# Performance work log

Measured on AMD Instinct MI355X. Metric: run time of the kernel, lower is better.

Reference implementation:

```python
import jax, jax.numpy as jnp
import numpy as np

H = 2048       # hidden_states
T = 8192       # input sequence length
N_ACT = 4      # n_actions
IN = 3         # num_sensors / LSTM input_size


def _uniform(k, shape, scale):
    return jax.random.uniform(k, shape, jnp.float32, -scale, scale)


def setup_inputs() -> dict:
    key = jax.random.key(0)
    ks = jax.random.split(key, 12)
    s = 1.0 / np.sqrt(H)  # torch LSTM/Linear default init scale
    return {
        "x": jax.random.normal(ks[0], (T, IN), jnp.float32),
        "last_dist": jax.random.uniform(ks[1], (), jnp.float32),
        "last_heading": jax.random.uniform(ks[2], (), jnp.float32),
        "W_ih": _uniform(ks[3], (4 * H, IN), s),
        "W_hh": _uniform(ks[4], (4 * H, H), s),
        "b_ih": _uniform(ks[5], (4 * H,), s),
        "b_hh": _uniform(ks[6], (4 * H,), s),
        "W1": _uniform(ks[7], (H, 4 * H), 1.0 / np.sqrt(4 * H)),
        "b1": _uniform(ks[8], (H,), 1.0 / np.sqrt(4 * H)),
        "W2": _uniform(ks[9], (4, H), s),
        "b2": _uniform(ks[10], (4,), s),
    }


def _lstm_cell(x_gates, h, c, W_hh, b):
    # x_gates: precomputed x @ W_ih.T contribution, shape (..., 4H)
    gates = x_gates + h @ W_hh.T + b
    i, f, g, o = jnp.split(gates, 4, axis=-1)  # torch gate order i,f,g,o
    c_new = jax.nn.sigmoid(f) * c + jax.nn.sigmoid(i) * jnp.tanh(g)
    h_new = jax.nn.sigmoid(o) * jnp.tanh(c_new)
    return h_new, c_new


def reference(x, last_dist, last_heading, W_ih, W_hh, b_ih, b_hh, W1, b1, W2, b2):
    h = W_hh.shape[1]
    b = b_ih + b_hh
    # --- run LSTM over the observation sequence (batch=1, unbatched vectors) ---
    x_gates = x @ W_ih.T  # (T, 4H), hoisted out of the scan
    h0 = jnp.zeros((h,), x.dtype)
    c0 = jnp.zeros((h,), x.dtype)

    def step(carry, xg):
        hh, cc = carry
        hh, cc = _lstm_cell(xg, hh, cc, W_hh, b)
        return (hh, cc), None

    (hn, cn), _ = jax.lax.scan(step, (h0, c0), x_gates)

    # --- 4 single-step action rollouts, batched instead of a Python loop ---
    acts = jnp.arange(N_ACT, dtype=x.dtype)
    last_states = jnp.stack(
        [jnp.broadcast_to(last_dist, (N_ACT,)),
         jnp.broadcast_to(last_heading, (N_ACT,)),
         acts], axis=1)  # (4, 3)
    a_gates = last_states @ W_ih.T  # (4, 4H)
    h_acts, _ = _lstm_cell(a_gates, hn[None, :], cn[None, :], W_hh, b)  # (4, H)

    feat = h_acts.reshape(-1)  # cat(dim=1) + flatten -> (4H,)
    hid = jax.nn.relu(feat @ W1.T + b1)
    return hid @ W2.T + b2  # (4,)
```

## Files before the change

### kernel.cpp

```cpp
#include <hip/hip_runtime.h>
#include <stdint.h>
#include <stddef.h>

#define T_SEQ 8192
#define HDIM  2048
#define NB    256
#define NT    512

typedef unsigned long long u64;
typedef unsigned int u32x4 __attribute__((ext_vector_type(4)));

#define WS_ZERO_DWORDS 9216

__global__ void init_ws_kernel(uint32_t* ws) {
    int i = blockIdx.x * blockDim.x + threadIdx.x;
    if (i < WS_ZERO_DWORDS) ws[i] = 0u;
}

__device__ __forceinline__ float sigm(float xv) { return 1.0f / (1.0f + expf(-xv)); }

__global__ void __launch_bounds__(NT)
__attribute__((amdgpu_waves_per_eu(2, 2)))
policy_persistent(
    const float* __restrict__ x,
    const float* __restrict__ ldist,
    const float* __restrict__ lhead,
    const float* __restrict__ W_ih,
    const float* __restrict__ W_hh,
    const float* __restrict__ b_ih,
    const float* __restrict__ b_hh,
    const float* __restrict__ W1,
    const float* __restrict__ b1,
    const float* __restrict__ W2,
    const float* __restrict__ b2,
    float* __restrict__ out,
    int*   __restrict__ flags,
    u64*   __restrict__ hbt,
    float* __restrict__ feat,
    float* __restrict__ hid)
{
    const int w    = blockIdx.x;
    const int tid  = threadIdx.x;
    const int v    = tid >> 6;
    const int lane = tid & 63;
    const int r    = v * 4 + (lane >> 4);
    const int g    = lane & 15;
    const int q    = r >> 3;
    const int p    = r & 7;

    __shared__ float4 h_lds4[16 * 33];
    __shared__ float  gates_lds[128];
    __shared__ float  c_lds[8];
    __shared__ float  red_lds[8];
    __shared__ float  feat_lds[4 * HDIM];

    const int row = q * HDIM + 8 * w + p;

    float4 wreg[32];
    {
        const float4* wp = (const float4*)(W_hh + (size_t)row * HDIM) + g * 32;
#pragma unroll
        for (int i = 0; i < 32; ++i) {
            wreg[i] = wp[i];
            asm volatile("" : "+v"(wreg[i].x), "+v"(wreg[i].y),
                              "+v"(wreg[i].z), "+v"(wreg[i].w));
        }
    }
    const float brow = b_ih[row] + b_hh[row];
    const float wih0 = W_ih[row * 3 + 0];
    const float wih1 = W_ih[row * 3 + 1];
    const float wih2 = W_ih[row * 3 + 2];
    if (tid < 8) c_lds[tid] = 0.0f;

    for (int t = 0; t <= T_SEQ; ++t) {
        float xt0 = 0.f, xt1 = 0.f, xt2 = 0.f;
        if (t < T_SEQ) { xt0 = x[3 * t]; xt1 = x[3 * t + 1]; xt2 = x[3 * t + 2]; }

        if (v == 0) {
            const u64* base = hbt + (size_t)((t + 1) & 1) * HDIM;
            const u64* p0 = base + 8 * (size_t)lane;
            const u64* p1 = p0 + 512;
            const u64* p2 = p0 + 1024;
            const u64* p3 = p0 + 1536;
            const uint32_t want = (uint32_t)t;
            for (;;) {
                u64 a0, a1, a2, a3;
                asm volatile(
                    "global_load_dwordx2 %0, %4, off sc0 sc1\n\t"
                    "global_load_dwordx2 %1, %5, off sc0 sc1\n\t"
                    "global_load_dwordx2 %2, %6, off sc0 sc1\n\t"
                    "global_load_dwordx2 %3, %7, off sc0 sc1\n\t"
                    "s_waitcnt vmcnt(0)"
                    : "=&v"(a0), "=&v"(a1), "=&v"(a2), "=&v"(a3)
                    : "v"(p0), "v"(p1), "v"(p2), "v"(p3)
                    : "memory");
                if ((uint32_t)(a0 >> 32) == want && (uint32_t)(a1 >> 32) == want &&
                    (uint32_t)(a2 >> 32) == want && (uint32_t)(a3 >> 32) == want)
                    break;
                __builtin_amdgcn_s_sleep(1);
            }
        }
        __syncthreads();

        {
            const u64* hp = hbt + (size_t)((t + 1) & 1) * HDIM + (size_t)tid * 4;
            const uint32_t want = (uint32_t)t;
            u32x4 b0, b1;
            for (;;) {
                asm volatile(
                    "global_load_dwordx4 %0, %2, off sc0 sc1\n\t"
                    "global_load_dwordx4 %1, %2, off offset:16 sc0 sc1\n\t"
                    "s_waitcnt vmcnt(0)"
                    : "=&v"(b0), "=&v"(b1)
                    : "v"(hp)
                    : "memory");
                if (b0.y == want && b0.w == want && b1.y == want && b1.w == want)
                    break;
                __builtin_amdgcn_s_sleep(1);
            }
            h_lds4[(tid >> 5) * 33 + (tid & 31)] =
                make_float4(__uint_as_float(b0.x), __uint_as_float(b0.z),
                            __uint_as_float(b1.x), __uint_as_float(b1.z));
        }
        __syncthreads();

        float acc = 0.0f;
        {
            const float4* hb = &h_lds4[g * 33];
#pragma unroll
            for (int i = 0; i < 32; ++i) {
                float4 hv = hb[i];
                float4 wv = wreg[i];
                acc = fmaf(wv.x, hv.x, acc); acc = fmaf(wv.y, hv.y, acc);
                acc = fmaf(wv.z, hv.z, acc); acc = fmaf(wv.w, hv.w, acc);
            }
        }
        acc += __shfl_xor(acc, 1, 64);
        acc += __shfl_xor(acc, 2, 64);
        acc += __shfl_xor(acc, 4, 64);
        acc += __shfl_xor(acc, 8, 64);

        if (t < T_SEQ) {
            if (g == 0) {
                float xg = wih0 * xt0 + wih1 * xt1 + wih2 * xt2;
                gates_lds[q * 8 + p] = acc + brow + xg;
            }
            __syncthreads();
            if (v == 0 && lane < 8) {
                float ig = gates_lds[lane],      fg = gates_lds[8 + lane];
                float gg = gates_lds[16 + lane], og = gates_lds[24 + lane];
                float c0 = c_lds[lane];
                float cn = sigm(fg) * c0 + sigm(ig) * tanhf(gg);
                float hn = sigm(og) * tanhf(cn);
                c_lds[lane] = cn;
                u64 pk = ((u64)(uint32_t)(t + 1) << 32) | (u64)__float_as_uint(hn);
                __hip_atomic_store(hbt + (size_t)(t & 1) * HDIM + 8 * w + lane, pk,
                                   __ATOMIC_RELAXED, __HIP_MEMORY_SCOPE_AGENT);
            }
        } else {
            const float ld0 = *ldist, lh0 = *lhead;
            if (g == 0) {
#pragma unroll
                for (int a = 0; a < 4; ++a) {
                    float xg = wih0 * ld0 + wih1 * lh0 + wih2 * (float)a;
                    gates_lds[a * 32 + q * 8 + p] = acc + brow + xg;
                }
            }
            __syncthreads();
            if (v == 0) {
                if (lane < 8) {
                    float c0 = c_lds[lane];
#pragma unroll
                    for (int a = 0; a < 4; ++a) {
                        float ig = gates_lds[a * 32 + lane];
                        float fg = gates_lds[a * 32 + 8 + lane];
                        float gg = gates_lds[a * 32 + 16 + lane];
                        float og = gates_lds[a * 32 + 24 + lane];
                        float cn = sigm(fg) * c0 + sigm(ig) * tanhf(gg);
                        float hn = sigm(og) * tanhf(cn);
                        __hip_atomic_store(&feat[a * HDIM + 8 * w + lane], hn,
                                           __ATOMIC_RELAXED, __HIP_MEMORY_SCOPE_AGENT);
                    }
                }
                __threadfence();
                if (lane == 0)
                    __hip_atomic_store(&flags[w * 4], 1, __ATOMIC_RELAXED,
                                       __HIP_MEMORY_SCOPE_AGENT);
            }
        }
    }

    if (tid < 256) {
        while (__hip_atomic_load(&flags[tid * 4], __ATOMIC_RELAXED,
                                 __HIP_MEMORY_SCOPE_AGENT) < 1)
            __builtin_amdgcn_s_sleep(1);
    }
    __syncthreads();
    {
        const u64* f64 = (const u64*)feat;
        u64* fl64 = (u64*)feat_lds;
#pragma unroll
        for (int k = 0; k < 8; ++k) {
            u64 a = __hip_atomic_load(f64 + k * NT + tid, __ATOMIC_RELAXED,
                                      __HIP_MEMORY_SCOPE_AGENT);
            fl64[k * NT + tid] = a;
        }
    }
    __syncthreads();
    const float4* flds4 = (const float4*)feat_lds;
    for (int rr = 0; rr < 8; ++rr) {
        const int hrow = 8 * w + rr;
        const float4* Wrow4 = (const float4*)(W1 + (size_t)hrow * 4 * HDIM);
        float pacc = 0.0f;
#pragma unroll
        for (int s = 0; s < 4; ++s) {
            int idx = s * NT + tid;
            float4 wv = Wrow4[idx];
            float4 fv = flds4[idx];
            pacc = fmaf(wv.x, fv.x, pacc); pacc = fmaf(wv.y, fv.y, pacc);
            pacc = fmaf(wv.z, fv.z, pacc); pacc = fmaf(wv.w, fv.w, pacc);
        }
#pragma unroll
        for (int m = 1; m < 64; m <<= 1) pacc += __shfl_xor(pacc, m, 64);
        if (lane == 0) red_lds[v] = pacc;
        __syncthreads();
        if (tid == 0) {
            float s = b1[hrow];
#pragma unroll
            for (int k = 0; k < 8; ++k) s += red_lds[k];
            __hip_atomic_store(&hid[hrow], fmaxf(s, 0.0f), __ATOMIC_RELAXED,
                               __HIP_MEMORY_SCOPE_AGENT);
        }
        __syncthreads();
    }
    __threadfence();
    if (tid == 0)
        __hip_atomic_store(&flags[w * 4], 2, __ATOMIC_RELAXED,
                           __HIP_MEMORY_SCOPE_AGENT);

    if (w == 0) {
        if (tid < 256) {
            while (__hip_atomic_load(&flags[tid * 4], __ATOMIC_RELAXED,
                                     __HIP_MEMORY_SCOPE_AGENT) < 2)
                __builtin_amdgcn_s_sleep(1);
        }
        __syncthreads();
        float hv4[4];
        {
            const u64* h64 = (const u64*)hid;
            u64 a0 = __hip_atomic_load(h64 + 2 * tid,     __ATOMIC_RELAXED,
                                       __HIP_MEMORY_SCOPE_AGENT);
            u64 a1 = __hip_atomic_load(h64 + 2 * tid + 1, __ATOMIC_RELAXED,
                                       __HIP_MEMORY_SCOPE_AGENT);
            float2 f0 = *(float2*)&a0;
            float2 f1 = *(float2*)&a1;
            hv4[0] = f0.x; hv4[1] = f0.y; hv4[2] = f1.x; hv4[3] = f1.y;
        }
#pragma unroll
        for (int o = 0; o < 4; ++o) {
            float pv = 0.0f;
#pragma unroll
            for (int k = 0; k < 4; ++k)
                pv = fmaf(W2[o * HDIM + tid * 4 + k], hv4[k], pv);
#pragma unroll
            for (int m = 1; m < 64; m <<= 1) pv += __shfl_xor(pv, m, 64);
            if (lane == 0) red_lds[v] = pv;
            __syncthreads();
            if (tid == 0) {
                float s = b2[o];
#pragma unroll
                for (int k = 0; k < 8; ++k) s += red_lds[k];
                out[o] = s;
            }
            __syncthreads();
        }
    }
}

extern "C" void kernel_launch(void* const* d_in, const int* in_sizes, int n_in,
                              void* d_out, int out_size, void* d_ws, size_t ws_size,
                              hipStream_t stream) {
    const float* x     = (const float*)d_in[0];
    const float* ldist = (const float*)d_in[1];
    const float* lhead = (const float*)d_in[2];
    const float* W_ih  = (const float*)d_in[3];
    const float* W_hh  = (const float*)d_in[4];
    const float* b_ih  = (const float*)d_in[5];
    const float* b_hh  = (const float*)d_in[6];
    const float* W1    = (const float*)d_in[7];
    const float* b1    = (const float*)d_in[8];
    const float* W2    = (const float*)d_in[9];
    const float* b2    = (const float*)d_in[10];
    float* out = (float*)d_out;

    uint8_t* wsb = (uint8_t*)d_ws;
    int*   flags = (int*)wsb;
    u64*   hbt   = (u64*)(wsb + 4096);
    float* feat  = (float*)(wsb + 36864);
    float* hid   = (float*)(wsb + 69632);

    hipLaunchKernelGGL(init_ws_kernel, dim3(36), dim3(256), 0, stream, (uint32_t*)d_ws);

    void* args[] = {
        (void*)&x, (void*)&ldist, (void*)&lhead, (void*)&W_ih, (void*)&W_hh,
        (void*)&b_ih, (void*)&b_hh, (void*)&W1, (void*)&b1, (void*)&W2, (void*)&b2,
        (void*)&out, (void*)&flags, (void*)&hbt, (void*)&feat, (void*)&hid
    };
    hipError_t e = hipLaunchCooperativeKernel((void*)policy_persistent,
                                              dim3(NB), dim3(NT), args, 0, stream);
    if (e != hipSuccess) {
        hipLaunchKernelGGL(policy_persistent, dim3(NB), dim3(NT), 0, stream,
                           x, ldist, lhead, W_ih, W_hh, b_ih, b_hh, W1, b1, W2, b2,
                           out, flags, hbt, feat, hid);
    }
}
```

Before: 24.41 ms.

## Replicate hidden-state broadcast buffer into eight copies to spread polling traffic

Each block now polls its own replica of the double-buffered h/timestamp array, chosen by block index modulo the copy count. Each producer writes its 8 new h values into every replica using 64 lanes instead of 8. The goal is to spread the 256 blocks' spin-poll reads across different memory addresses and channels, cutting contention on one hot buffer. In exchange there are eight times as many stores per step, plus a larger workspace that must be zeroed; it falls back to a single copy when the workspace is too small.

```diff
diff --git a/kernel.cpp b/kernel.cpp
--- a/kernel.cpp
+++ b/kernel.cpp
@@ -10,11 +10,10 @@
 typedef unsigned long long u64;
 typedef unsigned int u32x4 __attribute__((ext_vector_type(4)));
 
-#define WS_ZERO_DWORDS 9216
-
-__global__ void init_ws_kernel(uint32_t* ws) {
+
+__global__ void init_ws_kernel(uint32_t* ws, int ndw) {
     int i = blockIdx.x * blockDim.x + threadIdx.x;
-    if (i < WS_ZERO_DWORDS) ws[i] = 0u;
+    if (i < ndw) ws[i] = 0u;
 }
 
 __device__ __forceinline__ float sigm(float xv) { return 1.0f / (1.0f + expf(-xv)); }
@@ -37,7 +36,8 @@
     int*   __restrict__ flags,
     u64*   __restrict__ hbt,
     float* __restrict__ feat,
-    float* __restrict__ hid)
+    float* __restrict__ hid,
+    int ncpy)
 {
     const int w    = blockIdx.x;
     const int tid  = threadIdx.x;
@@ -56,6 +56,8 @@
 
     const int row = q * HDIM + 8 * w + p;
 
+    u64* const hb = hbt + (size_t)(w & (ncpy - 1)) * 2 * HDIM;
+
     float4 wreg[32];
     {
         const float4* wp = (const float4*)(W_hh + (size_t)row * HDIM) + g * 32;
@@ -77,7 +79,7 @@
         if (t < T_SEQ) { xt0 = x[3 * t]; xt1 = x[3 * t + 1]; xt2 = x[3 * t + 2]; }
 
         if (v == 0) {
-            const u64* base = hbt + (size_t)((t + 1) & 1) * HDIM;
+            const u64* base = hb + (size_t)((t + 1) & 1) * HDIM;
             const u64* p0 = base + 8 * (size_t)lane;
             const u64* p1 = p0 + 512;
             const u64* p2 = p0 + 1024;
@@ -103,7 +105,7 @@
         __syncthreads();
 
         {
-            const u64* hp = hbt + (size_t)((t + 1) & 1) * HDIM + (size_t)tid * 4;
+            const u64* hp = hb + (size_t)((t + 1) & 1) * HDIM + (size_t)tid * 4;
             const uint32_t want = (uint32_t)t;
             u32x4 b0, b1;
             for (;;) {
@@ -126,10 +128,10 @@
 
         float acc = 0.0f;
         {
-            const float4* hb = &h_lds4[g * 33];
+            const float4* hb4 = &h_lds4[g * 33];
 #pragma unroll
             for (int i = 0; i < 32; ++i) {
-                float4 hv = hb[i];
+                float4 hv = hb4[i];
                 float4 wv = wreg[i];
                 acc = fmaf(wv.x, hv.x, acc); acc = fmaf(wv.y, hv.y, acc);
                 acc = fmaf(wv.z, hv.z, acc); acc = fmaf(wv.w, hv.w, acc);
@@ -146,16 +148,23 @@
                 gates_lds[q * 8 + p] = acc + brow + xg;
             }
             __syncthreads();
-            if (v == 0 && lane < 8) {
-                float ig = gates_lds[lane],      fg = gates_lds[8 + lane];
-                float gg = gates_lds[16 + lane], og = gates_lds[24 + lane];
-                float c0 = c_lds[lane];
-                float cn = sigm(fg) * c0 + sigm(ig) * tanhf(gg);
-                float hn = sigm(og) * tanhf(cn);
-                c_lds[lane] = cn;
-                u64 pk = ((u64)(uint32_t)(t + 1) << 32) | (u64)__float_as_uint(hn);
-                __hip_atomic_store(hbt + (size_t)(t & 1) * HDIM + 8 * w + lane, pk,
-                                   __ATOMIC_RELAXED, __HIP_MEMORY_SCOPE_AGENT);
+            if (v == 0) {
+                float hn = 0.0f;
+                if (lane < 8) {
+                    float ig = gates_lds[lane],      fg = gates_lds[8 + lane];
+                    float gg = gates_lds[16 + lane], og = gates_lds[24 + lane];
+                    float c0 = c_lds[lane];
+                    float cn = sigm(fg) * c0 + sigm(ig) * tanhf(gg);
+                    hn = sigm(og) * tanhf(cn);
+                    c_lds[lane] = cn;
+                }
+                float hj = __shfl(hn, lane & 7, 64);
+                if (lane < 8 * ncpy) {
+                    u64 pk = ((u64)(uint32_t)(t + 1) << 32) | (u64)__float_as_uint(hj);
+                    __hip_atomic_store(hbt + (size_t)(lane >> 3) * 2 * HDIM
+                                           + (size_t)(t & 1) * HDIM + 8 * w + (lane & 7),
+                                       pk, __ATOMIC_RELAXED, __HIP_MEMORY_SCOPE_AGENT);
+                }
             }
         } else {
             const float ld0 = *ldist, lh0 = *lhead;
@@ -294,23 +303,27 @@
     float* out = (float*)d_out;
 
     uint8_t* wsb = (uint8_t*)d_ws;
+    int ncpy = (ws_size >= (size_t)307200) ? 8 : 1;
     int*   flags = (int*)wsb;
     u64*   hbt   = (u64*)(wsb + 4096);
-    float* feat  = (float*)(wsb + 36864);
-    float* hid   = (float*)(wsb + 69632);
-
-    hipLaunchKernelGGL(init_ws_kernel, dim3(36), dim3(256), 0, stream, (uint32_t*)d_ws);
+    float* feat  = (float*)(wsb + 4096 + (size_t)ncpy * 32768);
+    float* hid   = (float*)(wsb + 4096 + (size_t)ncpy * 32768 + 32768);
+
+    int zero_dwords = (4096 + ncpy * 32768) / 4;
+    hipLaunchKernelGGL(init_ws_kernel, dim3((zero_dwords + 255) / 256), dim3(256),
+                       0, stream, (uint32_t*)d_ws, zero_dwords);
 
     void* args[] = {
         (void*)&x, (void*)&ldist, (void*)&lhead, (void*)&W_ih, (void*)&W_hh,
         (void*)&b_ih, (void*)&b_hh, (void*)&W1, (void*)&b1, (void*)&W2, (void*)&b2,
-        (void*)&out, (void*)&flags, (void*)&hbt, (void*)&feat, (void*)&hid
+        (void*)&out, (void*)&flags, (void*)&hbt, (void*)&feat, (void*)&hid,
+        (void*)&ncpy
     };
     hipError_t e = hipLaunchCooperativeKernel((void*)policy_persistent,
                                               dim3(NB), dim3(NT), args, 0, stream);
     if (e != hipSuccess) {
         hipLaunchKernelGGL(policy_persistent, dim3(NB), dim3(NT), 0, stream,
                            x, ldist, lhead, W_ih, W_hh, b_ih, b_hh, W1, b1, W2, b2,
-                           out, flags, hbt, feat, hid);
+                           out, flags, hbt, feat, hid, ncpy);
     }
 }
```

New measurement: 23.85 ms. -2.3%, faster.
